# Optimization experiments

Hardware: AMD Instinct MI355X
Metric: run time of the kernel (lower is better)

Reference implementation:

```python
import jax, jax.numpy as jnp
import numpy as np

RANK = 3
NUM_STEPS = 3
NUM_ENT = 40000
NUM_EMB = 24
NUM_OPS = 12
DIM = 128
HID = 128
BATCH = 128
NNZ = 300000


def _lstm_dir(x, Wih, Whh, bih, bhh, reverse=False):
    # x: (S, B, D); PyTorch gate order i, f, g, o
    B = x.shape[1]
    H = Whh.shape[1]
    def step(carry, xt):
        h, c = carry
        z = xt @ Wih.T + h @ Whh.T + bih + bhh  # (B, 4H)
        i, f, g, o = jnp.split(z, 4, axis=-1)
        c = jax.nn.sigmoid(f) * c + jax.nn.sigmoid(i) * jnp.tanh(g)
        h = jax.nn.sigmoid(o) * jnp.tanh(c)
        return (h, c), h
    init = (jnp.zeros((B, H), x.dtype), jnp.zeros((B, H), x.dtype))
    _, hs = jax.lax.scan(step, init, x, reverse=reverse)
    return hs  # (S, B, H)


def _spmm(memory, src, dst, val, num_ent):
    # memory: (B, E); edges (src -> dst): out[b, j] = sum_{e: dst[e]=j} memory[b, src[e]] * val[e]
    g = memory[:, src] * val[None, :]              # (B, nnz)
    out = jax.ops.segment_sum(g.T, dst, num_segments=num_ent)  # (E, B)
    return out.T


def setup_inputs() -> dict:
    key = jax.random.key(0)
    ks = jax.random.split(key, 16)
    inp = {
        'queries': jax.random.randint(ks[0], (BATCH,), 0, NUM_EMB),
        'heads': jax.random.randint(ks[1], (BATCH,), 0, NUM_ENT),
        'edge_src': jax.random.randint(ks[2], (NUM_OPS, NNZ), 0, NUM_ENT, dtype=jnp.int32),
        'edge_dst': jax.random.randint(ks[3], (NUM_OPS, NNZ), 0, NUM_ENT, dtype=jnp.int32),
        'edge_val': jax.random.uniform(ks[4], (NUM_OPS, NNZ), jnp.float32),
        'emb': jax.random.normal(ks[5], (NUM_EMB, DIM), jnp.float32) * 0.1,
        'Wih_f': jax.random.normal(ks[6], (RANK, 4 * HID, DIM), jnp.float32) * 0.1,
        'Whh_f': jax.random.normal(ks[7], (RANK, 4 * HID, HID), jnp.float32) * 0.1,
        'bih_f': jnp.zeros((RANK, 4 * HID), jnp.float32),
        'bhh_f': jnp.zeros((RANK, 4 * HID), jnp.float32),
        'Wih_b': jax.random.normal(ks[8], (RANK, 4 * HID, DIM), jnp.float32) * 0.1,
        'Whh_b': jax.random.normal(ks[9], (RANK, 4 * HID, HID), jnp.float32) * 0.1,
        'bih_b': jnp.zeros((RANK, 4 * HID), jnp.float32),
        'bhh_b': jnp.zeros((RANK, 4 * HID), jnp.float32),
        'W0': jax.random.normal(ks[10], (2 * HID, NUM_OPS + 1), jnp.float32) * 0.1,
        'b0': jnp.zeros((1, NUM_OPS + 1), jnp.float32),
    }
    return inp


def reference(queries, heads, edge_src, edge_dst, edge_val, emb,
              Wih_f, Whh_f, bih_f, bhh_f, Wih_b, Whh_b, bih_b, bhh_b, W0, b0):
    # query embedding replicated over time: (S, B, D)
    q = emb[queries]
    x = jnp.broadcast_to(q[None], (NUM_STEPS, q.shape[0], q.shape[1]))
    head_onehot = jax.nn.one_hot(heads, NUM_ENT, dtype=jnp.float32)  # (B, E)

    logits = jnp.zeros((q.shape[0], NUM_ENT), jnp.float32)
    for r in range(RANK):
        hf = _lstm_dir(x, Wih_f[r], Whh_f[r], bih_f[r], bhh_f[r], reverse=False)
        hb = _lstm_dir(x, Wih_b[r], Whh_b[r], bih_b[r], bhh_b[r], reverse=True)
        rnn_out = jnp.concatenate([hf, hb], axis=-1)          # (S, B, 2H)
        trans = rnn_out @ W0 + b0                             # (S, B, ops+1)
        attn = jax.nn.softmax(trans, axis=-1)
        attn = jnp.transpose(attn, (0, 2, 1))                 # (S, ops+1, B)

        memory = head_onehot                                  # (B, E)
        for t in range(NUM_STEPS):
            attn_t = attn[t]                                  # (ops+1, B)
            acc = memory * attn_t[-1][:, None]                # identity operator
            for op in range(NUM_OPS):
                prod = _spmm(memory, edge_src[op], edge_dst[op], edge_val[op], NUM_ENT)
                acc = acc + prod * attn_t[op][:, None]
            memory = acc
        norm = jnp.maximum(jnp.float32(1e-20), jnp.sum(memory, axis=1, keepdims=True))
        logits = logits + memory / norm
    return logits
```

## Files before the change

kernel.cpp:

```cpp
#include <hip/hip_runtime.h>

#define NENT 40000
#define NB 128
#define NQ 24
#define NOPS 12
#define EPO 300000
#define NTOT (NOPS * EPO)
#define NRANK 3
#define NPASS 8
#define CP 16
#define ECAP 160
#define SEG 5000

typedef float v4f __attribute__((ext_vector_type(4)));

__device__ __forceinline__ v4f shfl_xor4(v4f x, int m) {
    v4f r;
    r.x = __shfl_xor(x.x, m);
    r.y = __shfl_xor(x.y, m);
    r.z = __shfl_xor(x.z, m);
    r.w = __shfl_xor(x.w, m);
    return r;
}

__device__ __forceinline__ bool bittest(const unsigned* bm, int i) {
    return (bm[i >> 5] >> (i & 31)) & 1u;
}

__global__ void headmark_kernel(const int* __restrict__ heads, unsigned* __restrict__ bmH,
                                unsigned* __restrict__ bm2) {
    int h = heads[threadIdx.x];
    atomicOr(&bmH[h >> 5], 1u << (h & 31));
    atomicOr(&bm2[h >> 5], 1u << (h & 31));
}

__global__ void mark2_kernel(const int* __restrict__ src, const int* __restrict__ dst,
                             const unsigned* __restrict__ bmH, unsigned* __restrict__ bm2) {
    int i = blockIdx.x * 256 + threadIdx.x;
    if (i < NTOT) {
        int s = __builtin_nontemporal_load(&src[i]);
        if (bittest(bmH, s)) {
            int d = dst[i];
            atomicOr(&bm2[d >> 5], 1u << (d & 31));
        }
    }
}

__global__ void build_ell_kernel(const int* __restrict__ src, const int* __restrict__ dst,
                                 const float* __restrict__ val, const unsigned* __restrict__ bm2,
                                 int* __restrict__ fillD, int* __restrict__ fillS,
                                 int2* __restrict__ eD, int2* __restrict__ eS) {
    int i = blockIdx.x * 256 + threadIdx.x;
    if (i >= NTOT) return;
    int s = __builtin_nontemporal_load(&src[i]);
    int d = __builtin_nontemporal_load(&dst[i]);
    int v = __builtin_nontemporal_load((const int*)&val[i]);
    int op = i / EPO;
    int pd = atomicAdd(&fillD[d], 1);
    eD[(size_t)d * ECAP + pd] = make_int2(s | (op << 16), v);
    if (bittest(bm2, s)) {
        int ps = atomicAdd(&fillS[s], 1);
        eS[(size_t)s * ECAP + ps] = make_int2(d | (op << 16), v);
    }
}

__global__ void pad_kernel(int* __restrict__ fillD, int2* __restrict__ eD) {
    int j = blockIdx.x * 256 + threadIdx.x;
    if (j >= NENT) return;
    int l = fillD[j];
    int lp = (l + 15) & ~15;
    int2* row = eD + (size_t)j * ECAP;
    for (int k = l; k < lp; ++k) row[k] = make_int2(0, 0);
    fillD[j] = lp;
}

__global__ void lstm_all_kernel(const float* __restrict__ emb,
                                const float* __restrict__ Wih_f, const float* __restrict__ bih_f,
                                const float* __restrict__ bhh_f,
                                const float* __restrict__ Wih_b, const float* __restrict__ bih_b,
                                const float* __restrict__ bhh_b,
                                const float* __restrict__ Whh_f, const float* __restrict__ Whh_b,
                                float* __restrict__ hq) {
    int combo = blockIdx.x / NQ;
    int q = blockIdx.x % NQ;
    int dir = combo / 3, r = combo % 3;
    const float* Wih = (dir ? Wih_b : Wih_f) + r * 512 * 128;
    const float* bih = (dir ? bih_b : bih_f) + r * 512;
    const float* bhh = (dir ? bhh_b : bhh_f) + r * 512;
    const float* Whh = (dir ? Whh_b : Whh_f) + r * 512 * 128;
    __shared__ float x[128];
    __shared__ float h[128];
    int u = threadIdx.x;
    x[u] = emb[q * 128 + u];
    __syncthreads();
    float a0 = 0.f, a1 = 0.f, a2 = 0.f, a3 = 0.f;
    {
        const float* W0p = Wih + u * 128;
        const float* W1p = Wih + (128 + u) * 128;
        const float* W2p = Wih + (256 + u) * 128;
        const float* W3p = Wih + (384 + u) * 128;
        for (int d = 0; d < 128; ++d) {
            float xv = x[d];
            a0 = fmaf(xv, W0p[d], a0);
            a1 = fmaf(xv, W1p[d], a1);
            a2 = fmaf(xv, W2p[d], a2);
            a3 = fmaf(xv, W3p[d], a3);
        }
    }
    float zi0 = a0 + bih[u] + bhh[u];
    float zf0 = a1 + bih[128 + u] + bhh[128 + u];
    float zg0 = a2 + bih[256 + u] + bhh[256 + u];
    float zo0 = a3 + bih[384 + u] + bhh[384 + u];
    const float* Wi = Whh + u * 128;
    const float* Wf = Whh + (128 + u) * 128;
    const float* Wg = Whh + (256 + u) * 128;
    const float* Wo = Whh + (384 + u) * 128;
    float c = 0.f;
    h[u] = 0.f;
    for (int s = 0; s < 3; ++s) {
        __syncthreads();
        float b0v = 0.f, b1v = 0.f, b2v = 0.f, b3v = 0.f;
        for (int d = 0; d < 128; ++d) {
            float hv = h[d];
            b0v = fmaf(hv, Wi[d], b0v);
            b1v = fmaf(hv, Wf[d], b1v);
            b2v = fmaf(hv, Wg[d], b2v);
            b3v = fmaf(hv, Wo[d], b3v);
        }
        float ig = 1.f / (1.f + expf(-(zi0 + b0v)));
        float fg = 1.f / (1.f + expf(-(zf0 + b1v)));
        float gg = tanhf(zg0 + b2v);
        float og = 1.f / (1.f + expf(-(zo0 + b3v)));
        c = fg * c + ig * gg;
        float hn = og * tanhf(c);
        __syncthreads();
        h[u] = hn;
        hq[(size_t)((combo * 3 + s) * NQ + q) * 128 + u] = hn;
    }
}

__global__ void attnq_kernel(const float* __restrict__ hq, const float* __restrict__ W0,
                             const float* __restrict__ b0, float* __restrict__ attnq) {
    int r = blockIdx.x / 3, t = blockIdx.x % 3;
    __shared__ float W0s[256 * 13];
    for (int idx = threadIdx.x; idx < 256 * 13; idx += 32) W0s[idx] = W0[idx];
    __syncthreads();
    int q = threadIdx.x;
    if (q >= NQ) return;
    float acc[13];
    for (int k = 0; k < 13; ++k) acc[k] = b0[k];
    const float* hf = hq + (size_t)(((0 * 3 + r) * 3 + t) * NQ + q) * 128;
    const float* hb = hq + (size_t)(((1 * 3 + r) * 3 + (2 - t)) * NQ + q) * 128;
    for (int u = 0; u < 128; ++u) {
        float v = hf[u];
        for (int k = 0; k < 13; ++k) acc[k] = fmaf(v, W0s[u * 13 + k], acc[k]);
    }
    for (int u = 0; u < 128; ++u) {
        float v = hb[u];
        for (int k = 0; k < 13; ++k) acc[k] = fmaf(v, W0s[(128 + u) * 13 + k], acc[k]);
    }
    float m = acc[0];
    for (int k = 1; k < 13; ++k) m = fmaxf(m, acc[k]);
    float e[13];
    float sum = 0.f;
    for (int k = 0; k < 13; ++k) { e[k] = expf(acc[k] - m); sum += e[k]; }
    float inv = 1.f / sum;
    float* ao = attnq + (size_t)(r * 3 + t) * 13 * NQ;
    for (int k = 0; k < 13; ++k) ao[k * NQ + q] = e[k] * inv;
}

__global__ void expand_kernel(const int* __restrict__ queries, const float* __restrict__ attnq,
                              float* __restrict__ attn) {
    __shared__ int qs[128];
    if (threadIdx.x < 128) qs[threadIdx.x] = queries[threadIdx.x];
    __syncthreads();
    for (int idx = threadIdx.x; idx < 9 * 13 * 128; idx += 256) {
        int b = idx & 127, kk = idx >> 7;
        attn[idx] = attnq[kk * NQ + qs[b]];
    }
}

__global__ __launch_bounds__(256) void fused01_kernel(const int* __restrict__ heads,
                                                      const float* __restrict__ attn,
                                                      const int* __restrict__ fillS,
                                                      const int2* __restrict__ eS,
                                                      float* __restrict__ mem2) {
    __shared__ float acc3[3][SEG];
    __shared__ float c0s[3][13], c1s[3][13];
    int b = blockIdx.x;
    int seg = blockIdx.y;
    int base = seg * SEG;
    int tid = threadIdx.x;
    if (tid < 39) {
        int r = tid / 13, k = tid % 13;
        c0s[r][k] = attn[(size_t)((r * 3 + 0) * 13 + k) * 128 + b];
        c1s[r][k] = attn[(size_t)((r * 3 + 1) * 13 + k) * 128 + b];
    }
    for (int k = tid; k < 3 * SEG; k += 256) ((float*)acc3)[k] = 0.f;
    __syncthreads();
    int h = heads[b];
    int lenH = fillS[h];
    for (int ent = tid; ent < lenH + 1; ent += 256) {
        int i;
        float wv0, wv1, wv2;
        if (ent == 0) {
            i = h;
            wv0 = c0s[0][12]; wv1 = c0s[1][12]; wv2 = c0s[2][12];
        } else {
            int2 e = eS[(size_t)h * ECAP + ent - 1];
            i = e.x & 0xFFFF;
            float v = __int_as_float(e.y);
            int op = e.x >> 16;
            wv0 = v * c0s[0][op]; wv1 = v * c0s[1][op]; wv2 = v * c0s[2][op];
        }
        unsigned ti = (unsigned)(i - base);
        if (ti < SEG) {
            atomicAdd(&acc3[0][ti], c1s[0][12] * wv0);
            atomicAdd(&acc3[1][ti], c1s[1][12] * wv1);
            atomicAdd(&acc3[2][ti], c1s[2][12] * wv2);
        }
        int lenI = fillS[i];
        const int2* ei = eS + (size_t)i * ECAP;
        for (int f = 0; f < lenI; ++f) {
            int2 e2 = ei[f];
            unsigned t = (unsigned)((e2.x & 0xFFFF) - base);
            if (t < SEG) {
                float v2 = __int_as_float(e2.y);
                int op2 = e2.x >> 16;
                atomicAdd(&acc3[0][t], v2 * c1s[0][op2] * wv0);
                atomicAdd(&acc3[1][t], v2 * c1s[1][op2] * wv1);
                atomicAdd(&acc3[2][t], v2 * c1s[2][op2] * wv2);
            }
        }
    }
    __syncthreads();
    int p = b >> 4, c = b & 15;
#pragma unroll
    for (int r = 0; r < 3; ++r) {
        float* dst = mem2 + ((size_t)(r * NPASS + p) * NENT + base) * CP + c;
        for (int k = tid; k < SEG; k += 256) dst[(size_t)k * CP] = acc3[r][k];
    }
}

__global__ __launch_bounds__(256) void dense_kernel(const float* __restrict__ attn,
                                                    const int* __restrict__ fillD,
                                                    const int2* __restrict__ edgesD,
                                                    const float* __restrict__ in,
                                                    float* __restrict__ out,
                                                    float* __restrict__ normv) {
    int p = blockIdx.x;
    int r = blockIdx.z;
    __shared__ __align__(16) float cs[13 * 20];
    __shared__ float npart[4][16];
    int tid = threadIdx.x;
    if (tid < 13 * 16) {
        int op = tid >> 4, c0 = tid & 15;
        cs[op * 20 + c0] = attn[(size_t)((r * 3 + 2) * 13 + op) * 128 + p * CP + c0];
    }
    __syncthreads();
    int wave = tid >> 6, lane = tid & 63;
    int slot = lane >> 2;
    int cq4 = (lane & 3) * 4;
    int jw = blockIdx.y * 32 + wave * 8;
    const float* inr = in + (size_t)(r * NPASS + p) * NENT * CP;
    float* outr = out + (size_t)(r * NPASS + p) * NENT * CP;
    int lens[8];
#pragma unroll
    for (int i = 0; i < 8; ++i) lens[i] = fillD[jw + i];
    v4f cid = *(const v4f*)&cs[12 * 20 + cq4];
    v4f rsum = (v4f)0.f;
#pragma unroll
    for (int rr = 0; rr < 8; ++rr) {
        int j = jw + rr;
        int len = lens[rr];
        const int2* ed = edgesD + (size_t)j * ECAP;
        v4f a = (v4f)0.f;
        int i = slot;
        for (; i + 48 < len; i += 64) {
            int2 e0 = ed[i];
            int2 e1 = ed[i + 16];
            int2 e2 = ed[i + 32];
            int2 e3 = ed[i + 48];
            v4f g0 = *(const v4f*)(inr + (size_t)(e0.x & 0xFFFF) * CP + cq4);
            v4f g1 = *(const v4f*)(inr + (size_t)(e1.x & 0xFFFF) * CP + cq4);
            v4f g2 = *(const v4f*)(inr + (size_t)(e2.x & 0xFFFF) * CP + cq4);
            v4f g3 = *(const v4f*)(inr + (size_t)(e3.x & 0xFFFF) * CP + cq4);
            v4f c0 = *(const v4f*)&cs[(e0.x >> 16) * 20 + cq4];
            v4f c1 = *(const v4f*)&cs[(e1.x >> 16) * 20 + cq4];
            v4f c2 = *(const v4f*)&cs[(e2.x >> 16) * 20 + cq4];
            v4f c3 = *(const v4f*)&cs[(e3.x >> 16) * 20 + cq4];
            a += (__int_as_float(e0.y) * c0) * g0;
            a += (__int_as_float(e1.y) * c1) * g1;
            a += (__int_as_float(e2.y) * c2) * g2;
            a += (__int_as_float(e3.y) * c3) * g3;
        }
        for (; i < len; i += 16) {
            int2 e0 = ed[i];
            v4f g0 = *(const v4f*)(inr + (size_t)(e0.x & 0xFFFF) * CP + cq4);
            v4f c0 = *(const v4f*)&cs[(e0.x >> 16) * 20 + cq4];
            a += (__int_as_float(e0.y) * c0) * g0;
        }
        a += shfl_xor4(a, 4);
        a += shfl_xor4(a, 8);
        a += shfl_xor4(a, 16);
        a += shfl_xor4(a, 32);
        if (slot == 0) {
            v4f mi = *(const v4f*)(inr + (size_t)j * CP + cq4);
            v4f res = cid * mi + a;
            *(v4f*)(outr + (size_t)j * CP + cq4) = res;
            rsum += res;
        }
    }
    if (slot == 0) *(v4f*)&npart[wave][cq4] = rsum;
    __syncthreads();
    if (tid < 16) {
        float s = npart[0][tid] + npart[1][tid] + npart[2][tid] + npart[3][tid];
        atomicAdd(&normv[r * 128 + p * CP + tid], s);
    }
}

__global__ void final_kernel(const float* __restrict__ mem3, const float* __restrict__ normv,
                             float* __restrict__ out) {
    __shared__ float tile[32 * 129];
    __shared__ float rn[384];
    for (int idx = threadIdx.x; idx < 384; idx += 256)
        rn[idx] = 1.f / fmaxf(normv[idx], 1e-20f);
    __syncthreads();
    int j0 = blockIdx.x * 32;
    for (int p = 0; p < NPASS; ++p) {
        for (int it = 0; it < 2; ++it) {
            int lin = it * 256 + threadIdx.x;
            int jj = lin >> 4, c = lin & 15;
            int b = p * CP + c;
            float s = 0.f;
            for (int r = 0; r < 3; ++r)
                s += mem3[((size_t)(r * NPASS + p) * NENT + j0 + jj) * CP + c] * rn[r * 128 + b];
            tile[jj * 129 + b] = s;
        }
    }
    __syncthreads();
    for (int it = 0; it < 16; ++it) {
        int lin = it * 256 + threadIdx.x;
        int b = lin >> 5, jj = lin & 31;
        out[(size_t)b * NENT + j0 + jj] = tile[jj * 129 + b];
    }
}

extern "C" void kernel_launch(void* const* d_in, const int* in_sizes, int n_in,
                              void* d_out, int out_size, void* d_ws, size_t ws_size,
                              hipStream_t stream) {
    const int*   queries  = (const int*)d_in[0];
    const int*   heads    = (const int*)d_in[1];
    const int*   edge_src = (const int*)d_in[2];
    const int*   edge_dst = (const int*)d_in[3];
    const float* edge_val = (const float*)d_in[4];
    const float* emb      = (const float*)d_in[5];
    const float* Wih_f    = (const float*)d_in[6];
    const float* Whh_f    = (const float*)d_in[7];
    const float* bih_f    = (const float*)d_in[8];
    const float* bhh_f    = (const float*)d_in[9];
    const float* Wih_b    = (const float*)d_in[10];
    const float* Whh_b    = (const float*)d_in[11];
    const float* bih_b    = (const float*)d_in[12];
    const float* bhh_b    = (const float*)d_in[13];
    const float* W0       = (const float*)d_in[14];
    const float* b0       = (const float*)d_in[15];
    float* out = (float*)d_out;

    char* w = (char*)d_ws;
    size_t off = 0;
    auto alloc = [&](size_t bytes) -> void* {
        off = (off + 255) & ~(size_t)255;
        void* p = w + off;
        off += bytes;
        return p;
    };
    float* attnq  = (float*)alloc((size_t)9 * 13 * NQ * sizeof(float));
    float* attn   = (float*)alloc((size_t)9 * 13 * 128 * sizeof(float));
    float* hq     = (float*)alloc((size_t)6 * 3 * NQ * 128 * sizeof(float));
    unsigned* bmH = (unsigned*)alloc((2 * 1250 + 2 * NENT) * sizeof(int));
    unsigned* bm2 = bmH + 1250;
    int* fillD    = (int*)(bm2 + 1250);
    int* fillS    = fillD + NENT;
    int2*  eD     = (int2*)alloc((size_t)NENT * ECAP * sizeof(int2));
    float* mem2   = (float*)alloc((size_t)NRANK * NENT * NB * sizeof(float));
    float* mem3   = (float*)alloc((size_t)NRANK * NENT * NB * sizeof(float));
    int2*  eS     = (int2*)mem3;
    float* normv  = (float*)alloc((size_t)NRANK * NB * sizeof(float));

    int cooGrid = (NTOT + 255) / 256;

    hipMemsetAsync(bmH, 0, (2 * 1250 + 2 * NENT) * sizeof(int), stream);
    headmark_kernel<<<1, 128, 0, stream>>>(heads, bmH, bm2);
    mark2_kernel<<<cooGrid, 256, 0, stream>>>(edge_src, edge_dst, bmH, bm2);
    build_ell_kernel<<<cooGrid, 256, 0, stream>>>(edge_src, edge_dst, edge_val, bm2,
                                                  fillD, fillS, eD, eS);
    pad_kernel<<<(NENT + 255) / 256, 256, 0, stream>>>(fillD, eD);

    lstm_all_kernel<<<6 * NQ, 128, 0, stream>>>(emb, Wih_f, bih_f, bhh_f,
                                                Wih_b, bih_b, bhh_b, Whh_f, Whh_b, hq);
    attnq_kernel<<<9, 32, 0, stream>>>(hq, W0, b0, attnq);
    expand_kernel<<<1, 256, 0, stream>>>(queries, attnq, attn);

    hipMemsetAsync(normv, 0, NRANK * NB * sizeof(float), stream);
    {
        dim3 g(NB, NENT / SEG);
        fused01_kernel<<<g, 256, 0, stream>>>(heads, attn, fillS, eS, mem2);
    }
    {
        dim3 g(NPASS, NENT / 32, NRANK);
        dense_kernel<<<g, 256, 0, stream>>>(attn, fillD, eD, mem2, mem3, normv);
    }

    final_kernel<<<NENT / 32, 256, 0, stream>>>(mem3, normv, out);
}
```

Baseline: 1.281 ms.

## Stage ELL edge rows in LDS and reuse them across all three ranks

The dense kernel now loads 16 destination rows of ELL edges into shared memory once and processes all three ranks in one block, instead of re-reading the edge lists from global memory for each rank. Norm partial sums are spread over 8 sub-buffers with per-lane atomics to reduce contention, and final_kernel sums these sub-buffers. Edge-building stores use nontemporal stores. The cost is higher LDS use per block (about 20KB), which limits occupancy, and a serial copy loop over rows.

New measurement: 1.382 ms. 7.9% more time.

```diff
diff --git a/kernel.cpp b/kernel.cpp
--- a/kernel.cpp
+++ b/kernel.cpp
@@ -11,6 +11,7 @@
 #define CP 16
 #define ECAP 160
 #define SEG 5000
+#define NSUB 8
 
 typedef float v4f __attribute__((ext_vector_type(4)));
 
@@ -25,6 +26,11 @@
 
 __device__ __forceinline__ bool bittest(const unsigned* bm, int i) {
     return (bm[i >> 5] >> (i & 31)) & 1u;
+}
+
+__device__ __forceinline__ void nt_store_edge(int2* p, int lo, int hi) {
+    long pk = ((long)(unsigned)hi << 32) | (unsigned)lo;
+    __builtin_nontemporal_store(pk, (long*)p);
 }
 
 __global__ void headmark_kernel(const int* __restrict__ heads, unsigned* __restrict__ bmH,
@@ -57,10 +63,10 @@
     int v = __builtin_nontemporal_load((const int*)&val[i]);
     int op = i / EPO;
     int pd = atomicAdd(&fillD[d], 1);
-    eD[(size_t)d * ECAP + pd] = make_int2(s | (op << 16), v);
+    nt_store_edge(&eD[(size_t)d * ECAP + pd], s | (op << 16), v);
     if (bittest(bm2, s)) {
         int ps = atomicAdd(&fillS[s], 1);
-        eS[(size_t)s * ECAP + ps] = make_int2(d | (op << 16), v);
+        nt_store_edge(&eS[(size_t)s * ECAP + ps], d | (op << 16), v);
     }
 }
 
@@ -70,7 +76,7 @@
     int l = fillD[j];
     int lp = (l + 15) & ~15;
     int2* row = eD + (size_t)j * ECAP;
-    for (int k = l; k < lp; ++k) row[k] = make_int2(0, 0);
+    for (int k = l; k < lp; ++k) nt_store_edge(&row[k], 0, 0);
     fillD[j] = lp;
 }
 
@@ -247,84 +253,99 @@
                                                     const int2* __restrict__ edgesD,
                                                     const float* __restrict__ in,
                                                     float* __restrict__ out,
-                                                    float* __restrict__ normv) {
+                                                    float* __restrict__ normv2) {
     int p = blockIdx.x;
-    int r = blockIdx.z;
-    __shared__ __align__(16) float cs[13 * 20];
-    __shared__ float npart[4][16];
+    int jb = blockIdx.y * 16;
+    __shared__ int2 eld[16][ECAP];
+    __shared__ __align__(16) float cs[3][13 * 20];
     int tid = threadIdx.x;
-    if (tid < 13 * 16) {
-        int op = tid >> 4, c0 = tid & 15;
-        cs[op * 20 + c0] = attn[(size_t)((r * 3 + 2) * 13 + op) * 128 + p * CP + c0];
-    }
-    __syncthreads();
+    for (int idx = tid; idx < 3 * 13 * 16; idx += 256) {
+        int r = idx / 208, rest = idx % 208;
+        int op = rest >> 4, c0 = rest & 15;
+        cs[r][op * 20 + c0] = attn[(size_t)((r * 3 + 2) * 13 + op) * 128 + p * CP + c0];
+    }
     int wave = tid >> 6, lane = tid & 63;
     int slot = lane >> 2;
     int cq4 = (lane & 3) * 4;
-    int jw = blockIdx.y * 32 + wave * 8;
-    const float* inr = in + (size_t)(r * NPASS + p) * NENT * CP;
-    float* outr = out + (size_t)(r * NPASS + p) * NENT * CP;
-    int lens[8];
+    int jw = jb + wave * 4;
+    int lens[4];
 #pragma unroll
-    for (int i = 0; i < 8; ++i) lens[i] = fillD[jw + i];
-    v4f cid = *(const v4f*)&cs[12 * 20 + cq4];
-    v4f rsum = (v4f)0.f;
+    for (int t = 0; t < 4; ++t) lens[t] = fillD[jw + t];
+    for (int row = 0; row < 16; ++row) {
+        int n4 = fillD[jb + row] >> 1;
+        const int4* srcp = (const int4*)(edgesD + (size_t)(jb + row) * ECAP);
+        int4* dstp = (int4*)&eld[row][0];
+        for (int u = tid; u < n4; u += 256) dstp[u] = srcp[u];
+    }
+    __syncthreads();
+    int sub = blockIdx.y & (NSUB - 1);
+    for (int r = 0; r < 3; ++r) {
+        const float* inr = in + (size_t)(r * NPASS + p) * NENT * CP;
+        float* outr = out + (size_t)(r * NPASS + p) * NENT * CP;
+        const float* csr = cs[r];
+        v4f cid = *(const v4f*)&csr[12 * 20 + cq4];
+        v4f rsum = (v4f)0.f;
 #pragma unroll
-    for (int rr = 0; rr < 8; ++rr) {
-        int j = jw + rr;
-        int len = lens[rr];
-        const int2* ed = edgesD + (size_t)j * ECAP;
-        v4f a = (v4f)0.f;
-        int i = slot;
-        for (; i + 48 < len; i += 64) {
-            int2 e0 = ed[i];
-            int2 e1 = ed[i + 16];
-            int2 e2 = ed[i + 32];
-            int2 e3 = ed[i + 48];
-            v4f g0 = *(const v4f*)(inr + (size_t)(e0.x & 0xFFFF) * CP + cq4);
-            v4f g1 = *(const v4f*)(inr + (size_t)(e1.x & 0xFFFF) * CP + cq4);
-            v4f g2 = *(const v4f*)(inr + (size_t)(e2.x & 0xFFFF) * CP + cq4);
-            v4f g3 = *(const v4f*)(inr + (size_t)(e3.x & 0xFFFF) * CP + cq4);
-            v4f c0 = *(const v4f*)&cs[(e0.x >> 16) * 20 + cq4];
-            v4f c1 = *(const v4f*)&cs[(e1.x >> 16) * 20 + cq4];
-            v4f c2 = *(const v4f*)&cs[(e2.x >> 16) * 20 + cq4];
-            v4f c3 = *(const v4f*)&cs[(e3.x >> 16) * 20 + cq4];
-            a += (__int_as_float(e0.y) * c0) * g0;
-            a += (__int_as_float(e1.y) * c1) * g1;
-            a += (__int_as_float(e2.y) * c2) * g2;
-            a += (__int_as_float(e3.y) * c3) * g3;
-        }
-        for (; i < len; i += 16) {
-            int2 e0 = ed[i];
-            v4f g0 = *(const v4f*)(inr + (size_t)(e0.x & 0xFFFF) * CP + cq4);
-            v4f c0 = *(const v4f*)&cs[(e0.x >> 16) * 20 + cq4];
-            a += (__int_as_float(e0.y) * c0) * g0;
-        }
-        a += shfl_xor4(a, 4);
-        a += shfl_xor4(a, 8);
-        a += shfl_xor4(a, 16);
-        a += shfl_xor4(a, 32);
+        for (int t = 0; t < 4; ++t) {
+            int lenp = lens[t];
+            const int2* erow = eld[wave * 4 + t];
+            v4f a = (v4f)0.f;
+            int i = slot;
+            for (; i + 48 < lenp; i += 64) {
+                int2 e0 = erow[i];
+                int2 e1 = erow[i + 16];
+                int2 e2 = erow[i + 32];
+                int2 e3 = erow[i + 48];
+                v4f g0 = *(const v4f*)(inr + (size_t)(e0.x & 0xFFFF) * CP + cq4);
+                v4f g1 = *(const v4f*)(inr + (size_t)(e1.x & 0xFFFF) * CP + cq4);
+                v4f g2 = *(const v4f*)(inr + (size_t)(e2.x & 0xFFFF) * CP + cq4);
+                v4f g3 = *(const v4f*)(inr + (size_t)(e3.x & 0xFFFF) * CP + cq4);
+                v4f c0 = *(const v4f*)&csr[(e0.x >> 16) * 20 + cq4];
+                v4f c1 = *(const v4f*)&csr[(e1.x >> 16) * 20 + cq4];
+                v4f c2 = *(const v4f*)&csr[(e2.x >> 16) * 20 + cq4];
+                v4f c3 = *(const v4f*)&csr[(e3.x >> 16) * 20 + cq4];
+                a += (__int_as_float(e0.y) * c0) * g0;
+                a += (__int_as_float(e1.y) * c1) * g1;
+                a += (__int_as_float(e2.y) * c2) * g2;
+                a += (__int_as_float(e3.y) * c3) * g3;
+            }
+            for (; i < lenp; i += 16) {
+                int2 e0 = erow[i];
+                v4f g0 = *(const v4f*)(inr + (size_t)(e0.x & 0xFFFF) * CP + cq4);
+                v4f c0 = *(const v4f*)&csr[(e0.x >> 16) * 20 + cq4];
+                a += (__int_as_float(e0.y) * c0) * g0;
+            }
+            a += shfl_xor4(a, 4);
+            a += shfl_xor4(a, 8);
+            a += shfl_xor4(a, 16);
+            a += shfl_xor4(a, 32);
+            if (slot == 0) {
+                int j = jw + t;
+                v4f mi = *(const v4f*)(inr + (size_t)j * CP + cq4);
+                v4f res = cid * mi + a;
+                *(v4f*)(outr + (size_t)j * CP + cq4) = res;
+                rsum += res;
+            }
+        }
         if (slot == 0) {
-            v4f mi = *(const v4f*)(inr + (size_t)j * CP + cq4);
-            v4f res = cid * mi + a;
-            *(v4f*)(outr + (size_t)j * CP + cq4) = res;
-            rsum += res;
-        }
-    }
-    if (slot == 0) *(v4f*)&npart[wave][cq4] = rsum;
-    __syncthreads();
-    if (tid < 16) {
-        float s = npart[0][tid] + npart[1][tid] + npart[2][tid] + npart[3][tid];
-        atomicAdd(&normv[r * 128 + p * CP + tid], s);
-    }
-}
-
-__global__ void final_kernel(const float* __restrict__ mem3, const float* __restrict__ normv,
+            float* nv = normv2 + sub * 384 + r * 128 + p * CP + cq4;
+            atomicAdd(&nv[0], rsum.x);
+            atomicAdd(&nv[1], rsum.y);
+            atomicAdd(&nv[2], rsum.z);
+            atomicAdd(&nv[3], rsum.w);
+        }
+    }
+}
+
+__global__ void final_kernel(const float* __restrict__ mem3, const float* __restrict__ normv2,
                              float* __restrict__ out) {
     __shared__ float tile[32 * 129];
     __shared__ float rn[384];
-    for (int idx = threadIdx.x; idx < 384; idx += 256)
-        rn[idx] = 1.f / fmaxf(normv[idx], 1e-20f);
+    for (int idx = threadIdx.x; idx < 384; idx += 256) {
+        float s = 0.f;
+        for (int sub = 0; sub < NSUB; ++sub) s += normv2[sub * 384 + idx];
+        rn[idx] = 1.f / fmaxf(s, 1e-20f);
+    }
     __syncthreads();
     int j0 = blockIdx.x * 32;
     for (int p = 0; p < NPASS; ++p) {
@@ -386,7 +407,7 @@
     float* mem2   = (float*)alloc((size_t)NRANK * NENT * NB * sizeof(float));
     float* mem3   = (float*)alloc((size_t)NRANK * NENT * NB * sizeof(float));
     int2*  eS     = (int2*)mem3;
-    float* normv  = (float*)alloc((size_t)NRANK * NB * sizeof(float));
+    float* normv2 = (float*)alloc((size_t)NSUB * 384 * sizeof(float));
 
     int cooGrid = (NTOT + 255) / 256;
 
@@ -402,15 +423,15 @@
     attnq_kernel<<<9, 32, 0, stream>>>(hq, W0, b0, attnq);
     expand_kernel<<<1, 256, 0, stream>>>(queries, attnq, attn);
 
-    hipMemsetAsync(normv, 0, NRANK * NB * sizeof(float), stream);
+    hipMemsetAsync(normv2, 0, NSUB * 384 * sizeof(float), stream);
     {
         dim3 g(NB, NENT / SEG);
         fused01_kernel<<<g, 256, 0, stream>>>(heads, attn, fillS, eS, mem2);
     }
     {
-        dim3 g(NPASS, NENT / 32, NRANK);
-        dense_kernel<<<g, 256, 0, stream>>>(attn, fillD, eD, mem2, mem3, normv);
-    }
-
-    final_kernel<<<NENT / 32, 256, 0, stream>>>(mem3, normv, out);
-}
+        dim3 g(NPASS, NENT / 16);
+        dense_kernel<<<g, 256, 0, stream>>>(attn, fillD, eD, mem2, mem3, normv2);
+    }
+
+    final_kernel<<<NENT / 32, 256, 0, stream>>>(mem3, normv2, out);
+}
```
